# Kernel tuning notes

Measured on AMD Instinct MI355X. Metric: run time of the kernel, lower is better.

The kernel has to match this reference:

```python
import jax, jax.numpy as jnp
import numpy as np

C = 64
C8 = C // 8
B, H, W = 2, 96, 96


def setup_inputs() -> dict:
    key = jax.random.key(0)
    ks = jax.random.split(key, 7)
    s = 0.05
    return {
        "x": jax.random.normal(ks[0], (B, C, H, W), dtype=jnp.float32),
        "Wq": jax.random.normal(ks[1], (C8, C), dtype=jnp.float32) * s,
        "bq": jnp.zeros((C8,), dtype=jnp.float32),
        "Wk": jax.random.normal(ks[2], (C8, C), dtype=jnp.float32) * s,
        "bk": jnp.zeros((C8,), dtype=jnp.float32),
        "Wv": jax.random.normal(ks[3], (C, C), dtype=jnp.float32) * s,
        "bv": jnp.zeros((C,), dtype=jnp.float32),
        "gamma": jnp.zeros((1,), dtype=jnp.float32),
        "dyn": jnp.ones((1,), dtype=jnp.float32),
    }


def reference(x, Wq, bq, Wk, bk, Wv, bv, gamma, dyn):
    b, c, h, w = x.shape
    n = h * w
    xf = x.reshape(b, c, n)  # [B, C, N]
    # 1x1 convs are channel-mixing matmuls
    q = jnp.einsum("oc,bcn->bno", Wq, xf) + bq  # [B, N, C8]
    k = jnp.einsum("oc,bcn->bon", Wk, xf) + bk[None, :, None]  # [B, C8, N]
    energy = jnp.einsum("bno,bom->bnm", q, k)  # [B, N, N]
    attn = dyn * jax.nn.softmax(energy, axis=-1)  # dynamic_weights scaling
    v = jnp.einsum("oc,bcn->bon", Wv, xf) + bv[None, :, None]  # [B, C, N]
    # out[b,c,i] = sum_j v[b,c,j] * attn[b,i,j]  (bmm(V, attn^T))
    out = jnp.einsum("bcm,bnm->bcn", v, attn).reshape(b, c, h, w)
    return gamma * out + x
```

## Files before the change

### kernel.cpp

```cpp
#include <hip/hip_runtime.h>

#define NTOK  9216
#define NBAT  2

typedef __attribute__((ext_vector_type(8))) short bf16x8;
typedef __attribute__((ext_vector_type(4))) float f32x4;
typedef __attribute__((ext_vector_type(4))) unsigned int u32x4;
typedef __attribute__((ext_vector_type(2))) unsigned int u32x2;

#if __has_builtin(__builtin_amdgcn_exp2f)
#define EXP2(x) __builtin_amdgcn_exp2f(x)
#else
#define EXP2(x) exp2f(x)
#endif
#define L2E 1.4426950408889634f

__device__ __forceinline__ unsigned short f2bf(float x) {
  unsigned int u = __builtin_bit_cast(unsigned int, x);
  u += 0x7fffu + ((u >> 16) & 1u);
  return (unsigned short)(u >> 16);
}

__device__ __forceinline__ unsigned int pack_bf2(float lo, float hi) {
  unsigned int ulo = __builtin_bit_cast(unsigned int, lo) + 0x8000u;
  unsigned int uhi = __builtin_bit_cast(unsigned int, hi) + 0x8000u;
  return __builtin_amdgcn_perm(uhi, ulo, 0x07060302u);
}

__device__ __forceinline__ void pl32(unsigned int &a, unsigned int &b) {
#if __has_builtin(__builtin_amdgcn_permlane32_swap)
  u32x2 r = __builtin_amdgcn_permlane32_swap(a, b, false, false);
  a = r[0]; b = r[1];
#else
  asm("v_permlane32_swap_b32 %0, %1" : "+v"(a), "+v"(b));
#endif
}
__device__ __forceinline__ void pl16(unsigned int &a, unsigned int &b) {
#if __has_builtin(__builtin_amdgcn_permlane16_swap)
  u32x2 r = __builtin_amdgcn_permlane16_swap(a, b, false, false);
  a = r[0]; b = r[1];
#else
  asm("v_permlane16_swap_b32 %0, %1" : "+v"(a), "+v"(b));
#endif
}

__global__ __launch_bounds__(256) void qkv_proj(
    const float* __restrict__ x,
    const float* __restrict__ Wq, const float* __restrict__ bq,
    const float* __restrict__ Wk, const float* __restrict__ bk,
    const float* __restrict__ Wv, const float* __restrict__ bv,
    unsigned short* __restrict__ qg, unsigned short* __restrict__ kg,
    unsigned short* __restrict__ vg)
{
  __shared__ __align__(16) float xl[64 * 68];
  const int bid = blockIdx.x;
  const int rg  = bid % 5;
  const int t2  = bid / 5;
  const int nt  = t2 % 144;
  const int b   = t2 / 144;
  const int t   = threadIdx.x;
  const int lane = t & 63;
  const int n0  = nt * 64;

  #pragma unroll
  for (int kk = 0; kk < 4; kk++) {
    int p = t + kk * 256;
    int c = p >> 4, n4 = (p & 15) << 2;
    *(float4*)(&xl[c * 68 + n4]) =
        *(const float4*)(x + (size_t)(b * 64 + c) * NTOK + n0 + n4);
  }
  __syncthreads();

  const int g  = __builtin_amdgcn_readfirstlane(t >> 6);
  const int r0 = rg * 16 + g * 4;

  const float* wbase; const float* bias_p; int lr0;
  if (r0 < 8)       { wbase = Wq; bias_p = bq; lr0 = r0; }
  else if (r0 < 16) { wbase = Wk; bias_p = bk; lr0 = r0 - 8; }
  else              { wbase = Wv; bias_p = bv; lr0 = r0 - 16; }
  const float* w0 = wbase + lr0 * 64;

  float a0 = 0.f, a1 = 0.f, a2 = 0.f, a3 = 0.f;
  #pragma unroll 16
  for (int c = 0; c < 64; c++) {
    float xv = xl[c * 68 + lane];
    a0 = fmaf(w0[c],       xv, a0);
    a1 = fmaf(w0[64 + c],  xv, a1);
    a2 = fmaf(w0[128 + c], xv, a2);
    a3 = fmaf(w0[192 + c], xv, a3);
  }
  a0 += bias_p[lr0]; a1 += bias_p[lr0 + 1];
  a2 += bias_p[lr0 + 2]; a3 += bias_p[lr0 + 3];
  if (r0 < 8) { a0 *= L2E; a1 *= L2E; a2 *= L2E; a3 *= L2E; }

  const int n = n0 + lane;
  if (r0 < 16) {
    ushort4 o;
    o.x = f2bf(a0); o.y = f2bf(a1); o.z = f2bf(a2); o.w = f2bf(a3);
    unsigned short* dst = (r0 < 8) ? qg : kg;
    *(ushort4*)(dst + ((size_t)b * NTOK + n) * 8 + lr0) = o;
  } else {
    unsigned short* vt = vg + ((size_t)(b * 144 + nt) * 64) * 64;
    vt[(lr0    ) * 64 + lane] = f2bf(a0);
    vt[(lr0 + 1) * 64 + lane] = f2bf(a1);
    vt[(lr0 + 2) * 64 + lane] = f2bf(a2);
    vt[(lr0 + 3) * 64 + lane] = f2bf(a3);
  }
}

__global__ __launch_bounds__(256, 2) void flash_partial(
    const unsigned short* __restrict__ qg,
    const unsigned short* __restrict__ kg,
    const unsigned short* __restrict__ vg,
    float* __restrict__ opart, float* __restrict__ lpart)
{
  __shared__ __align__(16) float obuf[2 * 4224];
  __shared__ float l_s[4][64];

  const int bid  = blockIdx.x;
  const int jh   = bid & 1;
  const int t2   = bid >> 1;
  const int rt   = t2 % 144;
  const int b    = t2 / 144;
  const int tid  = threadIdx.x;
  const int w    = tid >> 6;
  const int lane = tid & 63;
  const int i16  = lane & 15;
  const int quad = lane >> 4;
  const int jbase = jh * 4608 + (w << 6);

  const unsigned short* __restrict__ vb = vg + (size_t)b * 64 * NTOK;
  const unsigned short* __restrict__ kb = kg + (size_t)b * NTOK * 8;
  const int koff  = i16 * 8;
  const int vtoff = i16 * 64 + quad * 8;

  bf16x8 qf[4] = {};
  if (quad == 0) {
    #pragma unroll
    for (int s = 0; s < 4; s++)
      qf[s] = *(const bf16x8*)(qg + ((size_t)b * NTOK + rt * 64 + s * 16 + i16) * 8);
  }

  f32x4 acc[4][4];
  #pragma unroll
  for (int s = 0; s < 4; s++)
    #pragma unroll
    for (int ct = 0; ct < 4; ct++) acc[s][ct] = (f32x4){0.f, 0.f, 0.f, 0.f};
  float lp[4] = {0.f, 0.f, 0.f, 0.f};
  const f32x4 z4 = {0.f, 0.f, 0.f, 0.f};

  #pragma unroll 1
  for (int it = 0; it < 36; ++it) {
    const int jp  = jbase + ((it >> 1) << 8);
    const int jlo = (it & 1) << 5;

    bf16x8 kf[2];
    #pragma unroll
    for (int jt = 0; jt < 2; jt++)
      kf[jt] = *(const bf16x8*)(kb + (jp + jlo + jt * 16) * 8 + koff);
    bf16x8 vf[4];
    #pragma unroll
    for (int ct = 0; ct < 4; ct++)
      vf[ct] = *(const bf16x8*)(vb + (((size_t)(jp + ct * 16)) << 6) + vtoff + jlo);

    #pragma unroll
    for (int s = 0; s < 4; s++) {
      f32x4 st[2];
      #pragma unroll
      for (int jt = 0; jt < 2; jt++)
        st[jt] = __builtin_amdgcn_mfma_f32_16x16x32_bf16(kf[jt], qf[s], z4, 0, 0, 0);
      unsigned int pw[4];
      float ps = 0.f;
      #pragma unroll
      for (int jt = 0; jt < 2; jt++) {
        float p0 = EXP2(st[jt][0]);
        float p1 = EXP2(st[jt][1]);
        float p2 = EXP2(st[jt][2]);
        float p3 = EXP2(st[jt][3]);
        ps += (p0 + p1) + (p2 + p3);
        pw[jt * 2]     = pack_bf2(p0, p1);
        pw[jt * 2 + 1] = pack_bf2(p2, p3);
      }
      lp[s] += ps;

      unsigned int a0 = pw[0], a1 = pw[1];
      unsigned int b0 = pw[2], b1 = pw[3];
      pl32(a0, b0); pl16(a0, b0);
      pl32(a1, b1); pl16(a1, b1);
      u32x4 f = {a0, a1, b0, b1};
      bf16x8 pf = __builtin_bit_cast(bf16x8, f);
      #pragma unroll
      for (int ct = 0; ct < 4; ct++)
        acc[s][ct] = __builtin_amdgcn_mfma_f32_16x16x32_bf16(vf[ct], pf, acc[s][ct], 0, 0, 0);
    }
  }

  #pragma unroll
  for (int s = 0; s < 4; s++) {
    lp[s] += __shfl_xor(lp[s], 16);
    lp[s] += __shfl_xor(lp[s], 32);
  }
  if (quad == 0) {
    #pragma unroll
    for (int s = 0; s < 4; s++) l_s[w][s * 16 + i16] = lp[s];
  }

  if (w >= 2) {
    float* dst = &obuf[(w - 2) * 4224];
    #pragma unroll
    for (int s = 0; s < 4; s++)
      #pragma unroll
      for (int ct = 0; ct < 4; ct++)
        #pragma unroll
        for (int r = 0; r < 4; r++)
          dst[(ct * 16 + quad * 4 + r) * 66 + s * 16 + i16] = acc[s][ct][r];
  }
  __syncthreads();
  if (w < 2) {
    float* t = &obuf[w * 4224];
    #pragma unroll
    for (int s = 0; s < 4; s++)
      #pragma unroll
      for (int ct = 0; ct < 4; ct++)
        #pragma unroll
        for (int r = 0; r < 4; r++) {
          int idx = (ct * 16 + quad * 4 + r) * 66 + s * 16 + i16;
          t[idx] += acc[s][ct][r];
        }
  }
  __syncthreads();

  float* ob = opart + (size_t)bid * 4096;
  #pragma unroll
  for (int e0 = 0; e0 < 16; e0++) {
    int e = tid + e0 * 256, c = e >> 6, r = e & 63;
    ob[e] = obuf[c * 66 + r] + obuf[4224 + c * 66 + r];
  }
  if (tid < 64)
    lpart[(size_t)bid * 64 + tid] =
        (l_s[0][tid] + l_s[1][tid]) + (l_s[2][tid] + l_s[3][tid]);
}

__global__ __launch_bounds__(256) void reduce_ep(
    const float* __restrict__ x,
    const float* __restrict__ opart, const float* __restrict__ lpart,
    const float* __restrict__ gamma_p, const float* __restrict__ dyn_p,
    float* __restrict__ y)
{
  const int bid = blockIdx.x;
  const int b = bid / 144, rt = bid % 144;
  const int tid = threadIdx.x;
  const float gs = gamma_p[0] * dyn_p[0];
  const float* o0 = opart + (size_t)(bid * 2) * 4096;
  const float* o1 = o0 + 4096;
  const float* l0 = lpart + (size_t)(bid * 2) * 64;
  const float* l1 = l0 + 64;
  #pragma unroll
  for (int e0 = 0; e0 < 16; e0++) {
    int e = tid + e0 * 256, c = e >> 6, r = e & 63;
    float L = l0[r] + l1[r];
    float O = o0[e] + o1[e];
    size_t a = (size_t)(b * 64 + c) * NTOK + rt * 64 + r;
    y[a] = gs * O / L + x[a];
  }
}

extern "C" void kernel_launch(void* const* d_in, const int* in_sizes, int n_in,
                              void* d_out, int out_size, void* d_ws, size_t ws_size,
                              hipStream_t stream) {
  const float* x     = (const float*)d_in[0];
  const float* Wq    = (const float*)d_in[1];
  const float* bq    = (const float*)d_in[2];
  const float* Wk    = (const float*)d_in[3];
  const float* bk    = (const float*)d_in[4];
  const float* Wv    = (const float*)d_in[5];
  const float* bv    = (const float*)d_in[6];
  const float* gamma = (const float*)d_in[7];
  const float* dyn   = (const float*)d_in[8];
  float* y = (float*)d_out;

  unsigned short* qg = (unsigned short*)d_ws;
  unsigned short* kg = qg + (size_t)NBAT * NTOK * 8;
  unsigned short* vg = kg + (size_t)NBAT * NTOK * 8;
  float* opart = (float*)(vg + (size_t)NBAT * 64 * NTOK);
  float* lpart = opart + (size_t)576 * 4096;

  qkv_proj<<<NBAT * 144 * 5, 256, 0, stream>>>(x, Wq, bq, Wk, bk, Wv, bv, qg, kg, vg);
  flash_partial<<<NBAT * 144 * 2, 256, 0, stream>>>(qg, kg, vg, opart, lpart);
  reduce_ep<<<NBAT * 144, 256, 0, stream>>>(x, opart, lpart, gamma, dyn, y);
}
```

Before: 147.4 us.

## Double query tile per block and split keys four ways for K/V reuse

Each flash_partial block now processes 128 query rows instead of 64 and covers a quarter of the key range instead of half. Each K/V fragment loaded from global memory therefore feeds twice as many MFMAs, which halves K/V traffic per unit of work. The cost is doubled accumulator registers (acc[8][4]), which may reduce occupancy or cause spills, plus a two-pass shared-memory reduction and a four-way partial merge in reduce_ep with larger partial buffers.

```diff
diff --git a/kernel.cpp b/kernel.cpp
--- a/kernel.cpp
+++ b/kernel.cpp
@@ -115,42 +115,42 @@
     float* __restrict__ opart, float* __restrict__ lpart)
 {
   __shared__ __align__(16) float obuf[2 * 4224];
-  __shared__ float l_s[4][64];
+  __shared__ float l_s[4][128];
 
   const int bid  = blockIdx.x;
-  const int jh   = bid & 1;
-  const int t2   = bid >> 1;
-  const int rt   = t2 % 144;
-  const int b    = t2 / 144;
+  const int jq   = bid & 3;
+  const int t2   = bid >> 2;
+  const int rt   = t2 % 72;
+  const int b    = t2 / 72;
   const int tid  = threadIdx.x;
   const int w    = tid >> 6;
   const int lane = tid & 63;
   const int i16  = lane & 15;
   const int quad = lane >> 4;
-  const int jbase = jh * 4608 + (w << 6);
+  const int jbase = jq * 2304 + (w << 6);
 
   const unsigned short* __restrict__ vb = vg + (size_t)b * 64 * NTOK;
   const unsigned short* __restrict__ kb = kg + (size_t)b * NTOK * 8;
   const int koff  = i16 * 8;
   const int vtoff = i16 * 64 + quad * 8;
 
-  bf16x8 qf[4] = {};
+  bf16x8 qf[8] = {};
   if (quad == 0) {
     #pragma unroll
-    for (int s = 0; s < 4; s++)
-      qf[s] = *(const bf16x8*)(qg + ((size_t)b * NTOK + rt * 64 + s * 16 + i16) * 8);
-  }
-
-  f32x4 acc[4][4];
-  #pragma unroll
-  for (int s = 0; s < 4; s++)
+    for (int s = 0; s < 8; s++)
+      qf[s] = *(const bf16x8*)(qg + ((size_t)b * NTOK + rt * 128 + s * 16 + i16) * 8);
+  }
+
+  f32x4 acc[8][4];
+  #pragma unroll
+  for (int s = 0; s < 8; s++)
     #pragma unroll
     for (int ct = 0; ct < 4; ct++) acc[s][ct] = (f32x4){0.f, 0.f, 0.f, 0.f};
-  float lp[4] = {0.f, 0.f, 0.f, 0.f};
+  float lp[8] = {0.f, 0.f, 0.f, 0.f, 0.f, 0.f, 0.f, 0.f};
   const f32x4 z4 = {0.f, 0.f, 0.f, 0.f};
 
   #pragma unroll 1
-  for (int it = 0; it < 36; ++it) {
+  for (int it = 0; it < 18; ++it) {
     const int jp  = jbase + ((it >> 1) << 8);
     const int jlo = (it & 1) << 5;
 
@@ -164,7 +164,7 @@
       vf[ct] = *(const bf16x8*)(vb + (((size_t)(jp + ct * 16)) << 6) + vtoff + jlo);
 
     #pragma unroll
-    for (int s = 0; s < 4; s++) {
+    for (int s = 0; s < 8; s++) {
       f32x4 st[2];
       #pragma unroll
       for (int jt = 0; jt < 2; jt++)
@@ -196,48 +196,51 @@
   }
 
   #pragma unroll
-  for (int s = 0; s < 4; s++) {
+  for (int s = 0; s < 8; s++) {
     lp[s] += __shfl_xor(lp[s], 16);
     lp[s] += __shfl_xor(lp[s], 32);
   }
   if (quad == 0) {
     #pragma unroll
-    for (int s = 0; s < 4; s++) l_s[w][s * 16 + i16] = lp[s];
-  }
-
-  if (w >= 2) {
-    float* dst = &obuf[(w - 2) * 4224];
-    #pragma unroll
-    for (int s = 0; s < 4; s++)
-      #pragma unroll
-      for (int ct = 0; ct < 4; ct++)
+    for (int s = 0; s < 8; s++) l_s[w][s * 16 + i16] = lp[s];
+  }
+
+  float* ob = opart + (size_t)bid * 8192;
+  #pragma unroll
+  for (int p = 0; p < 2; p++) {
+    if (p) __syncthreads();
+    if (w >= 2) {
+      float* dst = &obuf[(w - 2) * 4224];
+      #pragma unroll
+      for (int s4 = 0; s4 < 4; s4++)
         #pragma unroll
-        for (int r = 0; r < 4; r++)
-          dst[(ct * 16 + quad * 4 + r) * 66 + s * 16 + i16] = acc[s][ct][r];
-  }
-  __syncthreads();
-  if (w < 2) {
-    float* t = &obuf[w * 4224];
-    #pragma unroll
-    for (int s = 0; s < 4; s++)
-      #pragma unroll
-      for (int ct = 0; ct < 4; ct++)
+        for (int ct = 0; ct < 4; ct++)
+          #pragma unroll
+          for (int r = 0; r < 4; r++)
+            dst[(ct * 16 + quad * 4 + r) * 66 + s4 * 16 + i16] = acc[p * 4 + s4][ct][r];
+    }
+    __syncthreads();
+    if (w < 2) {
+      float* t = &obuf[w * 4224];
+      #pragma unroll
+      for (int s4 = 0; s4 < 4; s4++)
         #pragma unroll
-        for (int r = 0; r < 4; r++) {
-          int idx = (ct * 16 + quad * 4 + r) * 66 + s * 16 + i16;
-          t[idx] += acc[s][ct][r];
-        }
-  }
-  __syncthreads();
-
-  float* ob = opart + (size_t)bid * 4096;
-  #pragma unroll
-  for (int e0 = 0; e0 < 16; e0++) {
-    int e = tid + e0 * 256, c = e >> 6, r = e & 63;
-    ob[e] = obuf[c * 66 + r] + obuf[4224 + c * 66 + r];
-  }
-  if (tid < 64)
-    lpart[(size_t)bid * 64 + tid] =
+        for (int ct = 0; ct < 4; ct++)
+          #pragma unroll
+          for (int r = 0; r < 4; r++) {
+            int idx = (ct * 16 + quad * 4 + r) * 66 + s4 * 16 + i16;
+            t[idx] += acc[p * 4 + s4][ct][r];
+          }
+    }
+    __syncthreads();
+    #pragma unroll
+    for (int e0 = 0; e0 < 16; e0++) {
+      int e = tid + e0 * 256, c = e >> 6, r = e & 63;
+      ob[c * 128 + p * 64 + r] = obuf[c * 66 + r] + obuf[4224 + c * 66 + r];
+    }
+  }
+  if (tid < 128)
+    lpart[(size_t)bid * 128 + tid] =
         (l_s[0][tid] + l_s[1][tid]) + (l_s[2][tid] + l_s[3][tid]);
 }
 
@@ -248,19 +251,20 @@
     float* __restrict__ y)
 {
   const int bid = blockIdx.x;
-  const int b = bid / 144, rt = bid % 144;
+  const int h  = bid & 1;
+  const int t  = bid >> 1;
+  const int rt = t % 72, b = t / 72;
   const int tid = threadIdx.x;
   const float gs = gamma_p[0] * dyn_p[0];
-  const float* o0 = opart + (size_t)(bid * 2) * 4096;
-  const float* o1 = o0 + 4096;
-  const float* l0 = lpart + (size_t)(bid * 2) * 64;
-  const float* l1 = l0 + 64;
+  const float* o0 = opart + (size_t)(t * 4) * 8192;
+  const float* l0 = lpart + (size_t)(t * 4) * 128;
   #pragma unroll
   for (int e0 = 0; e0 < 16; e0++) {
-    int e = tid + e0 * 256, c = e >> 6, r = e & 63;
-    float L = l0[r] + l1[r];
-    float O = o0[e] + o1[e];
-    size_t a = (size_t)(b * 64 + c) * NTOK + rt * 64 + r;
+    int e = tid + e0 * 256, c = e >> 6, r = (e & 63) + h * 64;
+    float L = (l0[r] + l0[128 + r]) + (l0[256 + r] + l0[384 + r]);
+    float O = (o0[c * 128 + r]         + o0[8192 + c * 128 + r])
+            + (o0[16384 + c * 128 + r] + o0[24576 + c * 128 + r]);
+    size_t a = (size_t)(b * 64 + c) * NTOK + rt * 128 + r;
     y[a] = gs * O / L + x[a];
   }
 }
@@ -283,9 +287,9 @@
   unsigned short* kg = qg + (size_t)NBAT * NTOK * 8;
   unsigned short* vg = kg + (size_t)NBAT * NTOK * 8;
   float* opart = (float*)(vg + (size_t)NBAT * 64 * NTOK);
-  float* lpart = opart + (size_t)576 * 4096;
+  float* lpart = opart + (size_t)576 * 8192;
 
   qkv_proj<<<NBAT * 144 * 5, 256, 0, stream>>>(x, Wq, bq, Wk, bk, Wv, bv, qg, kg, vg);
-  flash_partial<<<NBAT * 144 * 2, 256, 0, stream>>>(qg, kg, vg, opart, lpart);
-  reduce_ep<<<NBAT * 144, 256, 0, stream>>>(x, opart, lpart, gamma, dyn, y);
-}
+  flash_partial<<<NBAT * 72 * 4, 256, 0, stream>>>(qg, kg, vg, opart, lpart);
+  reduce_ep<<<NBAT * 72 * 2, 256, 0, stream>>>(x, opart, lpart, gamma, dyn, y);
+}
```

After: 146.7 us. Within noise of the previous version (-0.5%).
